# Performance work log

Hardware: AMD Instinct MI355X
Metric: run time of the kernel (lower is better)

Reference implementation:

```python
import jax, jax.numpy as jnp
import numpy as np

N_NEURONS = 4096

def setup_inputs() -> dict:
    key = jax.random.key(0)
    k1, = jax.random.split(key, 1)
    W_rec = 0.1 * jax.random.normal(k1, (N_NEURONS, N_NEURONS), dtype=jnp.float32)
    h0 = jnp.zeros((N_NEURONS,), dtype=jnp.float32)
    return {"W_rec": W_rec, "h0": h0, "n_steps": 4096}


def reference(W_rec, h0, n_steps):
    n = W_rec.shape[0]
    half = n // 2

    def step(h, _):
        h = jnp.tanh(W_rec @ h)                # [n] matvec + tanh
        action = jnp.tanh(jnp.mean(h[:half]))  # scalar readout
        return h, action

    _, actions = jax.lax.scan(step, h0, None, length=n_steps)
    return actions  # [n_steps]
```

## Files before the change

### kernel.cpp

```cpp
#include <hip/hip_runtime.h>


#define N 4096
#define HALF 2048
#define BLOCKS 256
#define TPB 1024
#define RPB 16
#define HWORDS (N / 2)

#define WS_FLAGS 0
#define WS_HA    4096
#define WS_HB    8192
#define WS_HC    12288
#define WS_HD    16384
#define WS_ACC   20480
#define WS_PART  24576

typedef unsigned u32x4 __attribute__((ext_vector_type(4)));

#if defined(__has_builtin)
#if __has_builtin(__builtin_amdgcn_fdot2_f32_bf16)
#define HAVE_DOT2 1
typedef __bf16 bf16x2 __attribute__((ext_vector_type(2)));
#endif
#endif
#ifndef HAVE_DOT2
#define HAVE_DOT2 0
#endif

__device__ __forceinline__ float agent_ld(const float* p) {
    return __hip_atomic_load(p, __ATOMIC_RELAXED, __HIP_MEMORY_SCOPE_AGENT);
}
__device__ __forceinline__ void agent_st(float* p, float v) {
    __hip_atomic_store(p, v, __ATOMIC_RELAXED, __HIP_MEMORY_SCOPE_AGENT);
}
__device__ __forceinline__ unsigned agent_ldu(const unsigned* p) {
    return __hip_atomic_load(p, __ATOMIC_RELAXED, __HIP_MEMORY_SCOPE_AGENT);
}
__device__ __forceinline__ void agent_stu(unsigned* p, unsigned v) {
    __hip_atomic_store(p, v, __ATOMIC_RELAXED, __HIP_MEMORY_SCOPE_AGENT);
}
__device__ __forceinline__ unsigned long long agent_ldu64(const unsigned long long* p) {
    return __hip_atomic_load(p, __ATOMIC_RELAXED, __HIP_MEMORY_SCOPE_AGENT);
}

__device__ __forceinline__ float tanh_fast(float x) {
    x = fminf(fmaxf(x, -15.0f), 15.0f);
    float e = __expf(2.0f * x);
    return (e - 1.0f) / (e + 1.0f);
}

__device__ __forceinline__ unsigned bf16_rne(float x) {
    unsigned u = __float_as_uint(x);
    return (u + 0x7FFFu + ((u >> 16) & 1u)) >> 16;
}
__device__ __forceinline__ float bf_lo(unsigned d) { return __uint_as_float(d << 16); }
__device__ __forceinline__ float bf_hi(unsigned d) { return __uint_as_float(d & 0xFFFF0000u); }

__device__ __forceinline__ float dot2bf(unsigned wp, unsigned hp, float c) {
#if HAVE_DOT2
    return __builtin_amdgcn_fdot2_f32_bf16(__builtin_bit_cast(bf16x2, wp),
                                           __builtin_bit_cast(bf16x2, hp),
                                           c, false);
#else
    c = fmaf(bf_lo(wp), bf_lo(hp), c);
    c = fmaf(bf_hi(wp), bf_hi(hp), c);
    return c;
#endif
}

__global__ void rnn_init(const float* __restrict__ h0, float* __restrict__ ws, int n_out) {
    int i = blockIdx.x * blockDim.x + threadIdx.x;
    if (i < BLOCKS * 16) agent_stu((unsigned*)ws + WS_FLAGS + i, 0u);
    if (i < n_out) agent_st(ws + WS_ACC + i, 0.0f);
    if (i < HWORDS) {
        unsigned d = bf16_rne(h0[2*i]) | (bf16_rne(h0[2*i+1]) << 16);
        agent_stu((unsigned*)ws + WS_HA + i, ~d);
        agent_stu((unsigned*)ws + WS_HB + i, 0u);
        agent_stu((unsigned*)ws + WS_HC + i, 0u);
        agent_stu((unsigned*)ws + WS_HD + i, 0u);
    }
}

__global__ void __launch_bounds__(TPB, 4)
rnn_persistent(const float* __restrict__ W, const int* __restrict__ pns,
               float* __restrict__ out, float* __restrict__ ws, int big) {
    const int b    = blockIdx.x;
    const int t    = threadIdx.x;
    const int lane = t & 63;
    const int wave = t >> 6;

    __shared__ __align__(16) unsigned wl[32768];
    __shared__ __align__(16) unsigned hs[HWORDS];
    __shared__ float part[16];

    {
        const float* Wr = W + (size_t)(b * RPB + wave) * N;
#pragma unroll
        for (int j = 0; j < 8; ++j) {
            const float* c0 = Wr + j * 512 + lane * 8;
            float4 va = *(const float4*)(c0);
            float4 vb = *(const float4*)(c0 + 4);
            u32x4 d;
            d.x = bf16_rne(va.x) | (bf16_rne(va.y) << 16);
            d.y = bf16_rne(va.z) | (bf16_rne(va.w) << 16);
            d.z = bf16_rne(vb.x) | (bf16_rne(vb.y) << 16);
            d.w = bf16_rne(vb.z) | (bf16_rne(vb.w) << 16);
            *(u32x4*)&wl[wave * 2048 + j * 256 + lane * 4] = d;
        }
    }
    __syncthreads();

    const int n_steps = *pns;

    unsigned* flags = (unsigned*)ws + WS_FLAGS;
    float* accum = ws + WS_ACC;
    float* parts = ws + WS_PART;

    unsigned* p0 = (unsigned*)ws + WS_HA;
    unsigned* p1 = (unsigned*)ws + WS_HB;
    unsigned* p2 = (unsigned*)ws + WS_HC;
    unsigned* p3 = (unsigned*)ws + WS_HD;

    for (int s = 0; s < n_steps; ++s) {
        unsigned lo, hi;
        {
            const unsigned long long* src = (const unsigned long long*)(p0 + 2 * t);
            unsigned spins = 0;
            for (;;) {
                unsigned long long q = agent_ldu64(src);
                lo = (unsigned)q; hi = (unsigned)(q >> 32);
                if (min(lo, hi) != 0u) break;
                __builtin_amdgcn_s_sleep(1);
                if (++spins > (1u << 22)) break;
            }
        }
        *(uint2*)&hs[2 * t] = make_uint2(~lo, ~hi);
        __syncthreads();

        if (t < 8) agent_stu(p2 + 8 * b + t, 0u);

        float acc = 0.0f;
        {
            const unsigned* wrow = wl + wave * 2048 + lane * 4;
            const unsigned* hrow = hs + lane * 4;
#pragma unroll
            for (int j = 0; j < 8; ++j) {
                u32x4 wd = *(const u32x4*)(wrow + j * 256);
                u32x4 hd = *(const u32x4*)(hrow + j * 256);
                acc = dot2bf(wd.x, hd.x, acc);
                acc = dot2bf(wd.y, hd.y, acc);
                acc = dot2bf(wd.z, hd.z, acc);
                acc = dot2bf(wd.w, hd.w, acc);
            }
        }
        acc += __shfl_down(acc, 32);
        acc += __shfl_down(acc, 16);
        acc += __shfl_down(acc, 8);
        acc += __shfl_down(acc, 4);
        acc += __shfl_down(acc, 2);
        acc += __shfl_down(acc, 1);
        if (lane == 0) part[wave] = tanh_fast(acc);
        __syncthreads();

        if (wave == 0) {
            if (lane < 8) {
                unsigned d = bf16_rne(part[2*lane]) | (bf16_rne(part[2*lane+1]) << 16);
                asm volatile("s_waitcnt vmcnt(0)" ::: "memory");
                agent_stu(p1 + 8 * b + lane, ~d);
            }
            float rv = (lane < RPB) ? part[lane] : 0.0f;
            rv += __shfl_down(rv, 8);
            rv += __shfl_down(rv, 4);
            rv += __shfl_down(rv, 2);
            rv += __shfl_down(rv, 1);
            if (lane == 0 && b < (HALF / RPB)) {
                if (big) agent_st(parts + (size_t)s * 128 + b, rv);
                else     atomicAdd(accum + s, rv);
            }
            if (!big && b == 0 && lane == 32 && s >= 2)
                out[s-2] = tanh_fast(agent_ld(accum + s - 2) * (1.0f / (float)HALF));
        }

        unsigned* tmp = p0; p0 = p1; p1 = p2; p2 = p3; p3 = tmp;
    }

    asm volatile("s_waitcnt vmcnt(0)" ::: "memory");
    __syncthreads();
    if (t == 0) agent_stu(flags + b * 16, 1u);
    if (t < BLOCKS) {
        unsigned spins = 0;
        while (agent_ldu(flags + t * 16) == 0u) {
            __builtin_amdgcn_s_sleep(1);
            if (++spins > (1u << 22)) break;
        }
    }
    __syncthreads();

    if (big) {
        for (int ss = b * 16 + wave; ss < n_steps; ss += BLOCKS * 16) {
            float v2 = agent_ld(parts + (size_t)ss * 128 + lane)
                     + agent_ld(parts + (size_t)ss * 128 + 64 + lane);
            v2 += __shfl_down(v2, 32);
            v2 += __shfl_down(v2, 16);
            v2 += __shfl_down(v2, 8);
            v2 += __shfl_down(v2, 4);
            v2 += __shfl_down(v2, 2);
            v2 += __shfl_down(v2, 1);
            if (lane == 0) out[ss] = tanh_fast(v2 * (1.0f / (float)HALF));
        }
    } else if (b == 0 && t == 0) {
        int k0 = (n_steps >= 2) ? n_steps - 2 : 0;
        for (int k = k0; k < n_steps; ++k)
            out[k] = tanh_fast(agent_ld(accum + k) * (1.0f / (float)HALF));
    }
}

extern "C" void kernel_launch(void* const* d_in, const int* in_sizes, int n_in,
                              void* d_out, int out_size, void* d_ws, size_t ws_size,
                              hipStream_t stream) {
    const float* W  = (const float*)d_in[0];
    const float* h0 = (const float*)d_in[1];
    const int*  pns = (const int*)d_in[2];
    float* out = (float*)d_out;
    float* ws  = (float*)d_ws;

    size_t need = ((size_t)WS_PART + (size_t)out_size * 128) * 4;
    int big = (ws_size >= need) ? 1 : 0;

    int n_init = out_size > N ? out_size : N;
    rnn_init<<<(n_init + 255) / 256, 256, 0, stream>>>(h0, ws, out_size);
    rnn_persistent<<<BLOCKS, TPB, 0, stream>>>(W, pns, out, ws, big);
}
```

Before: 11.59 ms.

## Split rows across wave groups with register-resident weights and DPP reductions

Reorganizes the per-block matvec so each group of four waves handles four rows and each wave covers a quarter of the columns. The LDS traffic for h drops because every h vector load is shared across four row accumulators. Weights are loaded into registers at the top of each step, ahead of the spin-wait, so those loads overlap with waiting on the previous step. Wave reductions use DPP row shifts instead of full shuffle chains, and a cross-wave combine in LDS precedes the tanh. This adds register pressure and an extra combine stage.

```diff
diff --git a/kernel.cpp b/kernel.cpp
--- a/kernel.cpp
+++ b/kernel.cpp
@@ -67,6 +67,19 @@
     c = fmaf(bf_hi(wp), bf_hi(hp), c);
     return c;
 #endif
+}
+
+__device__ __forceinline__ float dpp_scan16(float v) {
+    int x;
+    x = __builtin_amdgcn_update_dpp(0, __float_as_int(v), 0x111, 0xf, 0xf, true);
+    v += __int_as_float(x);
+    x = __builtin_amdgcn_update_dpp(0, __float_as_int(v), 0x112, 0xf, 0xf, true);
+    v += __int_as_float(x);
+    x = __builtin_amdgcn_update_dpp(0, __float_as_int(v), 0x114, 0xf, 0xf, true);
+    v += __int_as_float(x);
+    x = __builtin_amdgcn_update_dpp(0, __float_as_int(v), 0x118, 0xf, 0xf, true);
+    v += __int_as_float(x);
+    return v;
 }
 
 __global__ void rnn_init(const float* __restrict__ h0, float* __restrict__ ws, int n_out) {
@@ -89,24 +102,29 @@
     const int t    = threadIdx.x;
     const int lane = t & 63;
     const int wave = t >> 6;
+    const int g    = wave >> 2;
+    const int q    = wave & 3;
 
     __shared__ __align__(16) unsigned wl[32768];
     __shared__ __align__(16) unsigned hs[HWORDS];
-    __shared__ float part[16];
+    __shared__ __align__(16) float partc[64];
 
     {
-        const float* Wr = W + (size_t)(b * RPB + wave) * N;
 #pragma unroll
-        for (int j = 0; j < 8; ++j) {
-            const float* c0 = Wr + j * 512 + lane * 8;
-            float4 va = *(const float4*)(c0);
-            float4 vb = *(const float4*)(c0 + 4);
-            u32x4 d;
-            d.x = bf16_rne(va.x) | (bf16_rne(va.y) << 16);
-            d.y = bf16_rne(va.z) | (bf16_rne(va.w) << 16);
-            d.z = bf16_rne(vb.x) | (bf16_rne(vb.y) << 16);
-            d.w = bf16_rne(vb.z) | (bf16_rne(vb.w) << 16);
-            *(u32x4*)&wl[wave * 2048 + j * 256 + lane * 4] = d;
+        for (int r = 0; r < 4; ++r) {
+            const float* Wr = W + (size_t)(b * RPB + 4 * g + r) * N + q * 1024;
+#pragma unroll
+            for (int x = 0; x < 2; ++x) {
+                const float* c0 = Wr + x * 512 + lane * 8;
+                float4 va = *(const float4*)(c0);
+                float4 vb = *(const float4*)(c0 + 4);
+                u32x4 d;
+                d.x = bf16_rne(va.x) | (bf16_rne(va.y) << 16);
+                d.y = bf16_rne(va.z) | (bf16_rne(va.w) << 16);
+                d.z = bf16_rne(vb.x) | (bf16_rne(vb.y) << 16);
+                d.w = bf16_rne(vb.z) | (bf16_rne(vb.w) << 16);
+                *(u32x4*)&wl[wave * 2048 + r * 512 + x * 256 + lane * 4] = d;
+            }
         }
     }
     __syncthreads();
@@ -122,14 +140,24 @@
     unsigned* p2 = (unsigned*)ws + WS_HC;
     unsigned* p3 = (unsigned*)ws + WS_HD;
 
+    const unsigned* wbase = wl + wave * 2048 + lane * 4;
+    const unsigned* hbase = hs + q * 512 + lane * 4;
+
     for (int s = 0; s < n_steps; ++s) {
+        u32x4 w00 = *(const u32x4*)(wbase +    0), w01 = *(const u32x4*)(wbase + 256);
+        u32x4 w10 = *(const u32x4*)(wbase +  512), w11 = *(const u32x4*)(wbase + 768);
+        u32x4 w20 = *(const u32x4*)(wbase + 1024), w21 = *(const u32x4*)(wbase + 1280);
+        u32x4 w30 = *(const u32x4*)(wbase + 1536), w31 = *(const u32x4*)(wbase + 1792);
+        asm volatile("" : "+v"(w00), "+v"(w01), "+v"(w10), "+v"(w11),
+                          "+v"(w20), "+v"(w21), "+v"(w30), "+v"(w31) :: "memory");
+
         unsigned lo, hi;
         {
             const unsigned long long* src = (const unsigned long long*)(p0 + 2 * t);
             unsigned spins = 0;
             for (;;) {
-                unsigned long long q = agent_ldu64(src);
-                lo = (unsigned)q; hi = (unsigned)(q >> 32);
+                unsigned long long qv = agent_ldu64(src);
+                lo = (unsigned)qv; hi = (unsigned)(qv >> 32);
                 if (min(lo, hi) != 0u) break;
                 __builtin_amdgcn_s_sleep(1);
                 if (++spins > (1u << 22)) break;
@@ -140,36 +168,45 @@
 
         if (t < 8) agent_stu(p2 + 8 * b + t, 0u);
 
-        float acc = 0.0f;
-        {
-            const unsigned* wrow = wl + wave * 2048 + lane * 4;
-            const unsigned* hrow = hs + lane * 4;
+        u32x4 h0v = *(const u32x4*)(hbase + 0);
+        u32x4 h1v = *(const u32x4*)(hbase + 256);
+        float a0 = 0.f, a1 = 0.f, a2 = 0.f, a3 = 0.f;
 #pragma unroll
-            for (int j = 0; j < 8; ++j) {
-                u32x4 wd = *(const u32x4*)(wrow + j * 256);
-                u32x4 hd = *(const u32x4*)(hrow + j * 256);
-                acc = dot2bf(wd.x, hd.x, acc);
-                acc = dot2bf(wd.y, hd.y, acc);
-                acc = dot2bf(wd.z, hd.z, acc);
-                acc = dot2bf(wd.w, hd.w, acc);
-            }
-        }
-        acc += __shfl_down(acc, 32);
-        acc += __shfl_down(acc, 16);
-        acc += __shfl_down(acc, 8);
-        acc += __shfl_down(acc, 4);
-        acc += __shfl_down(acc, 2);
-        acc += __shfl_down(acc, 1);
-        if (lane == 0) part[wave] = tanh_fast(acc);
+        for (int e = 0; e < 4; ++e) {
+            a0 = dot2bf(w00[e], h0v[e], a0); a0 = dot2bf(w01[e], h1v[e], a0);
+            a1 = dot2bf(w10[e], h0v[e], a1); a1 = dot2bf(w11[e], h1v[e], a1);
+            a2 = dot2bf(w20[e], h0v[e], a2); a2 = dot2bf(w21[e], h1v[e], a2);
+            a3 = dot2bf(w30[e], h0v[e], a3); a3 = dot2bf(w31[e], h1v[e], a3);
+        }
+        a0 = dpp_scan16(a0); a1 = dpp_scan16(a1);
+        a2 = dpp_scan16(a2); a3 = dpp_scan16(a3);
+        a0 += __shfl_down(a0, 16); a1 += __shfl_down(a1, 16);
+        a2 += __shfl_down(a2, 16); a3 += __shfl_down(a3, 16);
+        a0 += __shfl_down(a0, 32); a1 += __shfl_down(a1, 32);
+        a2 += __shfl_down(a2, 32); a3 += __shfl_down(a3, 32);
+        if (lane == 15) {
+            *(float4*)&partc[wave * 4] = make_float4(a0, a1, a2, a3);
+        }
         __syncthreads();
 
         if (wave == 0) {
+            float hv = 0.0f;
+            if (lane < 16) {
+                int gg = lane >> 2, rr = lane & 3;
+                float s0 = partc[(gg * 4 + 0) * 4 + rr];
+                float s1 = partc[(gg * 4 + 1) * 4 + rr];
+                float s2 = partc[(gg * 4 + 2) * 4 + rr];
+                float s3 = partc[(gg * 4 + 3) * 4 + rr];
+                hv = tanh_fast((s0 + s1) + (s2 + s3));
+            }
+            float e0 = __shfl(hv, 2 * lane);
+            float e1 = __shfl(hv, 2 * lane + 1);
+            asm volatile("s_waitcnt vmcnt(0)" ::: "memory");
             if (lane < 8) {
-                unsigned d = bf16_rne(part[2*lane]) | (bf16_rne(part[2*lane+1]) << 16);
-                asm volatile("s_waitcnt vmcnt(0)" ::: "memory");
+                unsigned d = bf16_rne(e0) | (bf16_rne(e1) << 16);
                 agent_stu(p1 + 8 * b + lane, ~d);
             }
-            float rv = (lane < RPB) ? part[lane] : 0.0f;
+            float rv = (lane < 16) ? hv : 0.0f;
             rv += __shfl_down(rv, 8);
             rv += __shfl_down(rv, 4);
             rv += __shfl_down(rv, 2);
```

New measurement: 10.30 ms. 11.2% less time.
